# Kernel optimization log

Measured on AMD Instinct MI355X. Metric: run time of the kernel, lower is better.

The kernel has to match this reference:

```python
import jax, jax.numpy as jnp
import numpy as np

B, CIN, COUT, H, W = 8, 64, 64, 128, 128
DG = 1          # deformable groups
K = 9           # 3x3 kernel taps


def conv2d(x, w, b, pad):
    out = jax.lax.conv_general_dilated(
        x, w, window_strides=(1, 1), padding=[(pad, pad), (pad, pad)],
        dimension_numbers=("NCHW", "OIHW", "NCHW"))
    return out + b[None, :, None, None]


def deform_conv2d(x, offset, w, b, dg):
    """torchvision-style DeformConv2d, 3x3, stride 1, pad 1, zeros outside."""
    Bn, Cin, Hn, Wn = x.shape
    Cout = w.shape[0]
    Cg = Cin // dg
    # offset: [B, 2*dg*K, H, W] -> [B, dg, K, 2, H, W] (dy, dx per tap)
    off = offset.reshape(Bn, dg, K, 2, Hn, Wn)
    ky = jnp.repeat(jnp.arange(3) - 1, 3).astype(x.dtype)   # [K]
    kx = jnp.tile(jnp.arange(3) - 1, 3).astype(x.dtype)     # [K]
    base_y = ky[:, None, None] + jnp.arange(Hn, dtype=x.dtype)[None, :, None]  # [K,H,1]
    base_x = kx[:, None, None] + jnp.arange(Wn, dtype=x.dtype)[None, None, :]  # [K,1,W]
    py = base_y[None, None] + off[:, :, :, 0]   # [B,dg,K,H,W]
    px = base_x[None, None] + off[:, :, :, 1]   # [B,dg,K,H,W]

    xg = x.reshape(Bn, dg, Cg, Hn * Wn)         # grouped, flat spatial
    y0 = jnp.floor(py)
    x0 = jnp.floor(px)
    acc = jnp.zeros((Bn, dg, Cg, K * Hn * Wn), dtype=x.dtype)
    for dy in (0, 1):
        for dx in (0, 1):
            yc = y0 + dy
            xc = x0 + dx
            # bilinear corner weight; |py-yc| <= 1 for the 4 corners
            wgt = (1.0 - jnp.abs(py - yc)) * (1.0 - jnp.abs(px - xc))
            valid = (yc >= 0) & (yc < Hn) & (xc >= 0) & (xc < Wn)
            yi = jnp.clip(yc, 0, Hn - 1).astype(jnp.int32)
            xi = jnp.clip(xc, 0, Wn - 1).astype(jnp.int32)
            idx = (yi * Wn + xi).reshape(Bn, dg, 1, -1)          # [B,dg,1,K*H*W]
            v = jnp.take_along_axis(xg, idx, axis=3)             # [B,dg,Cg,K*H*W]
            acc = acc + v * (wgt * valid.astype(x.dtype)).reshape(Bn, dg, 1, -1)
    sampled = acc.reshape(Bn, dg, Cg, K, Hn, Wn)
    wk = w.reshape(Cout, dg, Cg, K)              # [Cout,dg,Cg,K]
    out = jnp.einsum("bgckhw,ogck->bohw", sampled, wk)
    return out + b[None, :, None, None]


def setup_inputs() -> dict:
    key = jax.random.key(0)
    ks = jax.random.split(key, 12)
    s = 0.05  # weight scale to keep activations bounded through the relu stack
    inp = {
        "x": jax.random.normal(ks[0], (B, CIN, H, W), jnp.float32),
        "of": jax.random.normal(ks[1], (B, 2, H, W), jnp.float32),
        "w1": jax.random.normal(ks[2], (CIN, CIN, 3, 3), jnp.float32) * s,
        "b1": jnp.zeros((CIN,), jnp.float32),
        "w2": jax.random.normal(ks[3], (CIN, CIN, 3, 3), jnp.float32) * s,
        "b2": jnp.zeros((CIN,), jnp.float32),
        "w3": jax.random.normal(ks[4], (CIN, CIN, 3, 3), jnp.float32) * s,
        "b3": jnp.zeros((CIN,), jnp.float32),
        "w_off": jax.random.normal(ks[5], (K * DG * 2, 2, 1, 1), jnp.float32) * 0.1,
        "b_off": jnp.zeros((K * DG * 2,), jnp.float32),
        "w_d": jax.random.normal(ks[6], (COUT, CIN, 3, 3), jnp.float32) * s,
        "b_d": jnp.zeros((COUT,), jnp.float32),
    }
    return inp


def reference(x, of, w1, b1, w2, b2, w3, b3, w_off, b_off, w_d, b_d):
    h = jax.nn.relu(conv2d(x, w1, b1, 1))
    h = jax.nn.relu(conv2d(h, w2, b2, 1))
    h = jax.nn.relu(conv2d(h, w3, b3, 1))
    offset = conv2d(of, w_off, b_off, 0)          # 1x1 offset conv -> [B,18*dg,H,W]
    return deform_conv2d(h, offset, w_d, b_d, DG)
```

## Files before the change

kernel.cpp:

```cpp
#include <hip/hip_runtime.h>
#include <math.h>

#define H_ 128
#define W_ 128
#define B_ 8
#define C_ 64
#define HW_ (H_*W_)
#define PW 130

typedef _Float16 half8 __attribute__((ext_vector_type(8)));
typedef _Float16 half4t __attribute__((ext_vector_type(4)));
typedef float f32x4 __attribute__((ext_vector_type(4)));

__device__ __forceinline__ int clampi(int v, int lo, int hi) {
    return v < lo ? lo : (v > hi ? hi : v);
}

__device__ __forceinline__ void stage16(const _Float16* g, _Float16* l) {
    __builtin_amdgcn_global_load_lds(
        (const __attribute__((address_space(1))) unsigned int*)g,
        (__attribute__((address_space(3))) unsigned int*)l, 16, 0, 0);
}

__global__ void wpack_kernel(const float* __restrict__ w1, const float* __restrict__ w2,
                             const float* __restrict__ w3, const float* __restrict__ wd,
                             _Float16* __restrict__ wp) {
    int t = blockIdx.x * 256 + threadIdx.x;
    if (t >= 4 * 4608) return;
    int set = t / 4608;
    int u   = t - set * 4608;
    const float* w = (set == 0) ? w1 : (set == 1) ? w2 : (set == 2) ? w3 : wd;
    int l  = u & 63;
    int mf = (u >> 6) & 3;
    int ch = (u >> 8) & 1;
    int kk = u >> 9;
    int co   = mf * 16 + (l & 15);
    int cin0 = ch * 32 + (l >> 4) * 8;
    half8 v;
#pragma unroll
    for (int j = 0; j < 8; ++j)
        v[j] = (_Float16)w[((co * C_) + cin0 + j) * 9 + kk];
    *(half8*)(wp + (size_t)set * 36864
                 + (size_t)(((ch * 9 + kk) * 4 + mf) * 64 + l) * 8) = v;
}

__global__ __launch_bounds__(256, 4)
void xpad_kernel(const float* __restrict__ x, _Float16* __restrict__ o) {
    __shared__ float lds[64][129];
    const int tid = threadIdx.x;
    const int b = blockIdx.x & 7, y = blockIdx.x >> 3;
    const int xr = tid & 127, cr = tid >> 7;
    const float* src = x + (size_t)b * C_ * HW_ + y * W_;
#pragma unroll
    for (int i = 0; i < 32; ++i) {
        int c = i * 2 + cr;
        lds[c][xr] = src[(size_t)c * HW_ + xr];
    }
    __syncthreads();
    const int px = tid & 127, hf = tid >> 7;
    _Float16* dst = o + ((size_t)((b * PW + y + 1) * PW) + px + 1) * C_ + hf * 32;
#pragma unroll
    for (int q = 0; q < 4; ++q) {
        half8 v;
#pragma unroll
        for (int j = 0; j < 8; ++j) v[j] = (_Float16)lds[hf * 32 + q * 8 + j][px];
        *(half8*)(dst + q * 8) = v;
    }
}

__global__ void zpad_kernel(_Float16* __restrict__ p0, _Float16* __restrict__ p1,
                            _Float16* __restrict__ p2) {
    int t = blockIdx.x * 256 + threadIdx.x;
    if (t >= 3 * B_ * 516) return;
    int which = t / (B_ * 516);
    int u = t - which * (B_ * 516);
    _Float16* o = (which == 0) ? p0 : (which == 1) ? p1 : p2;
    int b = u / 516, i = u % 516;
    int yp, xp;
    if (i < 260) { yp = (i < 130) ? 0 : (PW - 1); xp = i % 130; }
    else {
        int j = i - 260;
        if (j < 128) { xp = 0; yp = j + 1; }
        else         { xp = PW - 1; yp = j - 128 + 1; }
    }
    _Float16* dst = o + ((size_t)(b * PW + yp) * PW + xp) * C_;
    half8 z = (half8)(_Float16)0.f;
#pragma unroll
    for (int c8 = 0; c8 < 8; ++c8) *(half8*)(dst + c8 * 8) = z;
}

__global__ void offconv_kernel(const float* __restrict__ of,
                               const float* __restrict__ w,
                               const float* __restrict__ b,
                               float* __restrict__ out) {
    int bi = blockIdx.x & 7;
    int p  = (blockIdx.x >> 3) * 256 + threadIdx.x;
    float a0 = of[(bi * 2 + 0) * HW_ + p];
    float a1 = of[(bi * 2 + 1) * HW_ + p];
#pragma unroll
    for (int kk = 0; kk < 9; ++kk) {
        float dy = b[2 * kk]     + w[(2 * kk) * 2] * a0     + w[(2 * kk) * 2 + 1] * a1;
        float dx = b[2 * kk + 1] + w[(2 * kk + 1) * 2] * a0 + w[(2 * kk + 1) * 2 + 1] * a1;
        float2 v; v.x = dy; v.y = dx;
        *(float2*)(out + ((size_t)(bi * 9 + kk) * HW_ + p) * 2) = v;
    }
}

__global__ __launch_bounds__(1024, 1)
void conv3x3_mfma(const _Float16* __restrict__ in, const _Float16* __restrict__ wpk,
                  const float* __restrict__ bias, _Float16* __restrict__ outp) {
    __shared__ _Float16 Ash[9 * 4 * 64 * 8];
    __shared__ _Float16 Tile[6 * 4 * 130 * 8];
    const int tid = threadIdx.x;
    const int wv = tid >> 6, l = tid & 63;
    const int l15 = l & 15, lg = l >> 4;
    const int b  = blockIdx.x & 7;
    const int R  = (blockIdx.x >> 3) * 4;
    const int rowi = wv >> 2;
    const int xh = (wv & 3) * 32;

    f32x4 acc[4][2];
#pragma unroll
    for (int i = 0; i < 4; ++i)
#pragma unroll
        for (int j = 0; j < 2; ++j) acc[i][j] = (f32x4){0.f, 0.f, 0.f, 0.f};

    half8 bf0[2], bf1[2];

#define LOADB(BF, KK)                                                          \
    {                                                                          \
        _Pragma("unroll") for (int nf = 0; nf < 2; ++nf)                       \
            BF[nf] = *(const half8*)(Tile + (size_t)(((rowi + (KK) / 3) * 4 + lg) \
                          * 130 + xh + (KK) % 3 + nf * 16 + l15) * 8);         \
    }
#define MM(BF, KK)                                                             \
    {                                                                          \
        half8 af_[4];                                                          \
        _Pragma("unroll") for (int mf = 0; mf < 4; ++mf)                       \
            af_[mf] = *(const half8*)(Ash + (size_t)(((KK) * 4 + mf) * 64 + l) * 8); \
        _Pragma("unroll") for (int mf = 0; mf < 4; ++mf)                       \
            _Pragma("unroll") for (int nf = 0; nf < 2; ++nf)                   \
                acc[mf][nf] = __builtin_amdgcn_mfma_f32_16x16x32_f16(          \
                    af_[mf], BF[nf], acc[mf][nf], 0, 0, 0);                    \
    }

#pragma unroll
    for (int ch = 0; ch < 2; ++ch) {
        __syncthreads();
#pragma unroll
        for (int i = 0; i < 6; ++i) {
            int idx = i * 1024 + tid;
            if (idx < 2304) {
                stage16(wpk + (size_t)ch * 18432 + (size_t)idx * 8,
                        Ash + (size_t)idx * 8);
            } else if (idx < 5424) {
                int t   = idx - 2304;
                int dy  = t / 520;
                int rem = t - dy * 520;
                int pl  = rem / 130;
                int col = rem - pl * 130;
                stage16(in + ((size_t)((b * PW + R + dy) * PW) + col) * C_
                            + ch * 32 + pl * 8,
                        Tile + (size_t)t * 8);
            }
        }
        __syncthreads();

        LOADB(bf0, 0);
        LOADB(bf1, 1); MM(bf0, 0);
        LOADB(bf0, 2); MM(bf1, 1);
        LOADB(bf1, 3); MM(bf0, 2);
        LOADB(bf0, 4); MM(bf1, 3);
        LOADB(bf1, 5); MM(bf0, 4);
        LOADB(bf0, 6); MM(bf1, 5);
        LOADB(bf1, 7); MM(bf0, 6);
        LOADB(bf0, 8); MM(bf1, 7);
                       MM(bf0, 8);
    }
#undef LOADB
#undef MM

    _Float16* ob = outp + ((size_t)((b * PW + R + rowi + 1) * PW) + xh + 1) * C_;
#pragma unroll
    for (int mf = 0; mf < 4; ++mf) {
        const int co = mf * 16 + lg * 4;
        const float b0 = bias[co], b1 = bias[co + 1], b2 = bias[co + 2], b3 = bias[co + 3];
#pragma unroll
        for (int nf = 0; nf < 2; ++nf) {
            f32x4 v = acc[mf][nf];
            half4t h;
            h[0] = (_Float16)fmaxf(v[0] + b0, 0.f);
            h[1] = (_Float16)fmaxf(v[1] + b1, 0.f);
            h[2] = (_Float16)fmaxf(v[2] + b2, 0.f);
            h[3] = (_Float16)fmaxf(v[3] + b3, 0.f);
            *(half4t*)(ob + (nf * 16 + l15) * C_ + co) = h;
        }
    }
}

__global__ __launch_bounds__(1024, 1)
void deform_mfma(const _Float16* __restrict__ hin, const float* __restrict__ off,
                 const _Float16* __restrict__ wpk, const float* __restrict__ bias,
                 float* __restrict__ out) {
    __shared__ _Float16 Ash[9 * 4 * 64 * 8];
    __shared__ _Float16 Win[8 * 130 * 40];
    __shared__ _Float16 OffS[9 * 4 * 128 * 4];
    const int tid = threadIdx.x;
    const int wv = tid >> 6, l = tid & 63;
    const int l15 = l & 15, lg = l >> 4;
    const int b  = blockIdx.x & 7;
    const int R  = (blockIdx.x >> 3) * 4;
    const int r  = R + (wv >> 2);
    const int xh = (wv & 3) * 32;

    const _Float16* hb = hin + (size_t)b * PW * PW * C_;
    const float* offp = off + (size_t)b * 9 * HW_ * 2;

#pragma unroll
    for (int i = 0; i < 3; ++i) {
        int idx = i * 1024 + tid;
        if (idx < 2304) {
            int kk = idx >> 8, rowi = (idx >> 6) & 3, c = idx & 63;
            const _Float16* g = (const _Float16*)(offp
                + ((size_t)kk * HW_ + (R + rowi) * W_) * 2) + c * 8;
            stage16(g, OffS + (size_t)idx * 8);
        }
    }

    f32x4 acc[4][2];
#pragma unroll
    for (int i = 0; i < 4; ++i)
#pragma unroll
        for (int j = 0; j < 2; ++j) acc[i][j] = (f32x4){0.f, 0.f, 0.f, 0.f};

    half8 bf[2];

#define GATHB(KK, CH) do {                                                     \
    _Pragma("unroll") for (int nf = 0; nf < 2; ++nf) {                         \
        const int pxl = xh + nf * 16 + l15;                                    \
        float2 o2 = *(const float2*)(OffS +                                    \
            (size_t)((((KK) * 4 + (r - R)) << 7) + pxl) * 4);                  \
        float py = (float)(r + (KK) / 3 - 1) + o2.x;                           \
        float px = (float)(pxl + (KK) % 3 - 1) + o2.y;                         \
        float fy0 = floorf(py), fx0 = floorf(px);                              \
        float fy = py - fy0, fx = px - fx0;                                    \
        int iy0 = (int)fy0, ix0 = (int)fx0;                                    \
        int cy0 = clampi(iy0, -1, 128), cy1 = clampi(iy0 + 1, -1, 128);        \
        int px0 = clampi(ix0, -1, 128) + 1, px1 = clampi(ix0 + 1, -1, 128) + 1;\
        _Float16 w00 = (_Float16)((1.f - fy) * (1.f - fx));                    \
        _Float16 w01 = (_Float16)((1.f - fy) * fx);                            \
        _Float16 w10 = (_Float16)(fy * (1.f - fx));                            \
        _Float16 w11 = (_Float16)(fy * fx);                                    \
        half8 c0, c1, c2, c3;                                                  \
        int s0 = cy0 + 2 - R, s1 = cy1 + 2 - R;                                \
        if (__all((s0 >= 0) & (s1 <= 7))) {                                    \
            const _Float16* w0 = Win + (size_t)(s0 * 130) * 40 + lg * 8;       \
            const _Float16* w1 = Win + (size_t)(s1 * 130) * 40 + lg * 8;       \
            c0 = *(const half8*)(w0 + px0 * 40);                               \
            c1 = *(const half8*)(w0 + px1 * 40);                               \
            c2 = *(const half8*)(w1 + px0 * 40);                               \
            c3 = *(const half8*)(w1 + px1 * 40);                               \
        } else {                                                               \
            const _Float16* g0 = hb + (size_t)((cy0 + 1) * PW) * C_ + (CH) * 32 + lg * 8; \
            const _Float16* g1 = hb + (size_t)((cy1 + 1) * PW) * C_ + (CH) * 32 + lg * 8; \
            c0 = *(const half8*)(g0 + px0 * C_);                               \
            c1 = *(const half8*)(g0 + px1 * C_);                               \
            c2 = *(const half8*)(g1 + px0 * C_);                               \
            c3 = *(const half8*)(g1 + px1 * C_);                               \
        }                                                                      \
        bf[nf] = (c0 * w00 + c1 * w01) + (c2 * w10 + c3 * w11);                \
    }                                                                          \
} while (0)
#define MMT(KK) do {                                                           \
    half8 af0 = *(const half8*)(Ash + (size_t)(((KK) * 4 + 0) * 64 + l) * 8);  \
    half8 af1 = *(const half8*)(Ash + (size_t)(((KK) * 4 + 1) * 64 + l) * 8);  \
    half8 af2 = *(const half8*)(Ash + (size_t)(((KK) * 4 + 2) * 64 + l) * 8);  \
    half8 af3 = *(const half8*)(Ash + (size_t)(((KK) * 4 + 3) * 64 + l) * 8);  \
    _Pragma("unroll") for (int nf = 0; nf < 2; ++nf) {                         \
        acc[0][nf] = __builtin_amdgcn_mfma_f32_16x16x32_f16(af0, bf[nf], acc[0][nf], 0, 0, 0); \
        acc[1][nf] = __builtin_amdgcn_mfma_f32_16x16x32_f16(af1, bf[nf], acc[1][nf], 0, 0, 0); \
        acc[2][nf] = __builtin_amdgcn_mfma_f32_16x16x32_f16(af2, bf[nf], acc[2][nf], 0, 0, 0); \
        acc[3][nf] = __builtin_amdgcn_mfma_f32_16x16x32_f16(af3, bf[nf], acc[3][nf], 0, 0, 0); \
    }                                                                          \
} while (0)

#pragma unroll
    for (int ch = 0; ch < 2; ++ch) {
        __syncthreads();
#pragma unroll
        for (int i = 0; i < 3; ++i) {
            int idx = i * 1024 + tid;
            if (idx < 2304)
                stage16(wpk + (size_t)ch * 18432 + (size_t)idx * 8,
                        Ash + (size_t)idx * 8);
        }
#pragma unroll
        for (int i = 0; i < 6; ++i) {
            int idx = i * 1024 + tid;
            if (idx < 5200) {
                int s   = idx / 650;
                int rem = idx - s * 650;
                int c   = rem / 5;
                int q   = rem - c * 5;
                int prow = clampi(R - 1 + s, 0, 129);
                stage16(hb + ((size_t)(prow * PW) + c) * C_ + ch * 32 + (q < 4 ? q : 3) * 8,
                        Win + (size_t)idx * 8);
            }
        }
        __syncthreads();

        GATHB(0, ch); MMT(0);
        GATHB(1, ch); MMT(1);
        GATHB(2, ch); MMT(2);
        GATHB(3, ch); MMT(3);
        GATHB(4, ch); MMT(4);
        GATHB(5, ch); MMT(5);
        GATHB(6, ch); MMT(6);
        GATHB(7, ch); MMT(7);
        GATHB(8, ch); MMT(8);
    }
#undef GATHB
#undef MMT

    float* WF = (float*)Win;
    float* obase = out + (size_t)b * C_ * HW_;
#pragma unroll
    for (int p = 0; p < 4; ++p) {
        __syncthreads();
#pragma unroll
        for (int nf = 0; nf < 2; ++nf) {
            f32x4 v = acc[p][nf];
#pragma unroll
            for (int rr = 0; rr < 4; ++rr) {
                int co16 = lg * 4 + rr;
                WF[co16 * 512 + (r - R) * 128 + xh + nf * 16 + l15]
                    = v[rr] + bias[p * 16 + co16];
            }
        }
        __syncthreads();
#pragma unroll
        for (int i = 0; i < 2; ++i) {
            int g4   = i * 1024 + tid;
            int co16 = g4 >> 7;
            int q    = g4 & 127;
            int rr2  = q >> 5;
            int px4  = q & 31;
            f32x4 v = *(const f32x4*)&WF[g4 * 4];
            *(f32x4*)(obase + (size_t)(p * 16 + co16) * HW_ + (R + rr2) * W_ + px4 * 4) = v;
        }
    }
}

extern "C" void kernel_launch(void* const* d_in, const int* in_sizes, int n_in,
                              void* d_out, int out_size, void* d_ws, size_t ws_size,
                              hipStream_t stream) {
    const float* x     = (const float*)d_in[0];
    const float* of    = (const float*)d_in[1];
    const float* w1    = (const float*)d_in[2];
    const float* b1    = (const float*)d_in[3];
    const float* w2    = (const float*)d_in[4];
    const float* b2    = (const float*)d_in[5];
    const float* w3    = (const float*)d_in[6];
    const float* b3    = (const float*)d_in[7];
    const float* w_off = (const float*)d_in[8];
    const float* b_off = (const float*)d_in[9];
    const float* w_d   = (const float*)d_in[10];
    const float* b_d   = (const float*)d_in[11];
    float* out = (float*)d_out;

    char* base = (char*)d_ws;
    float*     offb = (float*)base;
    char* p = base + (size_t)B_ * 18 * HW_ * 4;
    _Float16* wpA = (_Float16*)p;
    _Float16* wp1 = wpA;
    _Float16* wp2 = wp1 + 36864;
    _Float16* wp3 = wp2 + 36864;
    _Float16* wpd = wp3 + 36864;
    p += 4 * 36864 * 2;
    _Float16* xp = (_Float16*)p; p += (size_t)B_ * PW * PW * C_ * 2;
    _Float16* hA = (_Float16*)p; p += (size_t)B_ * PW * PW * C_ * 2;
    _Float16* hB = (_Float16*)p;

    wpack_kernel<<<72, 256, 0, stream>>>(w1, w2, w3, w_d, wpA);
    zpad_kernel<<<(3 * B_ * 516 + 255) / 256, 256, 0, stream>>>(xp, hA, hB);
    xpad_kernel<<<H_ * B_, 256, 0, stream>>>(x, xp);
    offconv_kernel<<<(B_ * HW_) / 256, 256, 0, stream>>>(of, w_off, b_off, offb);

    conv3x3_mfma<<<256, 1024, 0, stream>>>(xp, wp1, b1, hA);
    conv3x3_mfma<<<256, 1024, 0, stream>>>(hA, wp2, b2, hB);
    conv3x3_mfma<<<256, 1024, 0, stream>>>(hB, wp3, b3, hA);
    deform_mfma<<<256, 1024, 0, stream>>>(hA, offb, wpd, b_d, out);
}
```

Baseline: 120.2 us.

## Merge prep kernels into one launch and halve conv block to 512 threads

The four preprocessing kernels (weight pack, pad zeroing, input transpose/pad, offset conv) are merged into a single launch that dispatches on block index. This removes three kernel launches and the gaps between them. Separately, the 3x3 conv kernel now runs 8 waves instead of 16, and each wave computes 64 output columns (4 N-fragments) rather than 32. That gives each wave more MFMA work per A-fragment load at the cost of higher register use and fewer waves to hide latency.

```diff
diff --git a/kernel.cpp b/kernel.cpp
--- a/kernel.cpp
+++ b/kernel.cpp
@@ -22,91 +22,92 @@
         (__attribute__((address_space(3))) unsigned int*)l, 16, 0, 0);
 }
 
-__global__ void wpack_kernel(const float* __restrict__ w1, const float* __restrict__ w2,
-                             const float* __restrict__ w3, const float* __restrict__ wd,
-                             _Float16* __restrict__ wp) {
-    int t = blockIdx.x * 256 + threadIdx.x;
-    if (t >= 4 * 4608) return;
-    int set = t / 4608;
-    int u   = t - set * 4608;
-    const float* w = (set == 0) ? w1 : (set == 1) ? w2 : (set == 2) ? w3 : wd;
-    int l  = u & 63;
-    int mf = (u >> 6) & 3;
-    int ch = (u >> 8) & 1;
-    int kk = u >> 9;
-    int co   = mf * 16 + (l & 15);
-    int cin0 = ch * 32 + (l >> 4) * 8;
-    half8 v;
-#pragma unroll
-    for (int j = 0; j < 8; ++j)
-        v[j] = (_Float16)w[((co * C_) + cin0 + j) * 9 + kk];
-    *(half8*)(wp + (size_t)set * 36864
-                 + (size_t)(((ch * 9 + kk) * 4 + mf) * 64 + l) * 8) = v;
-}
-
 __global__ __launch_bounds__(256, 4)
-void xpad_kernel(const float* __restrict__ x, _Float16* __restrict__ o) {
+void prep_kernel(const float* __restrict__ w1, const float* __restrict__ w2,
+                 const float* __restrict__ w3, const float* __restrict__ wd,
+                 _Float16* __restrict__ wp,
+                 _Float16* __restrict__ z0, _Float16* __restrict__ z1,
+                 _Float16* __restrict__ z2,
+                 const float* __restrict__ x,  _Float16* __restrict__ xp,
+                 const float* __restrict__ of, const float* __restrict__ wof,
+                 const float* __restrict__ bof, float* __restrict__ offb) {
     __shared__ float lds[64][129];
+    const int blk = blockIdx.x;
     const int tid = threadIdx.x;
-    const int b = blockIdx.x & 7, y = blockIdx.x >> 3;
-    const int xr = tid & 127, cr = tid >> 7;
-    const float* src = x + (size_t)b * C_ * HW_ + y * W_;
-#pragma unroll
-    for (int i = 0; i < 32; ++i) {
-        int c = i * 2 + cr;
-        lds[c][xr] = src[(size_t)c * HW_ + xr];
-    }
-    __syncthreads();
-    const int px = tid & 127, hf = tid >> 7;
-    _Float16* dst = o + ((size_t)((b * PW + y + 1) * PW) + px + 1) * C_ + hf * 32;
-#pragma unroll
-    for (int q = 0; q < 4; ++q) {
+
+    if (blk < 72) {
+        int t = blk * 256 + tid;
+        if (t >= 4 * 4608) return;
+        int set = t / 4608;
+        int u   = t - set * 4608;
+        const float* w = (set == 0) ? w1 : (set == 1) ? w2 : (set == 2) ? w3 : wd;
+        int l  = u & 63;
+        int mf = (u >> 6) & 3;
+        int ch = (u >> 8) & 1;
+        int kk = u >> 9;
+        int co   = mf * 16 + (l & 15);
+        int cin0 = ch * 32 + (l >> 4) * 8;
         half8 v;
 #pragma unroll
-        for (int j = 0; j < 8; ++j) v[j] = (_Float16)lds[hf * 32 + q * 8 + j][px];
-        *(half8*)(dst + q * 8) = v;
-    }
-}
-
-__global__ void zpad_kernel(_Float16* __restrict__ p0, _Float16* __restrict__ p1,
-                            _Float16* __restrict__ p2) {
-    int t = blockIdx.x * 256 + threadIdx.x;
-    if (t >= 3 * B_ * 516) return;
-    int which = t / (B_ * 516);
-    int u = t - which * (B_ * 516);
-    _Float16* o = (which == 0) ? p0 : (which == 1) ? p1 : p2;
-    int b = u / 516, i = u % 516;
-    int yp, xp;
-    if (i < 260) { yp = (i < 130) ? 0 : (PW - 1); xp = i % 130; }
-    else {
-        int j = i - 260;
-        if (j < 128) { xp = 0; yp = j + 1; }
-        else         { xp = PW - 1; yp = j - 128 + 1; }
-    }
-    _Float16* dst = o + ((size_t)(b * PW + yp) * PW + xp) * C_;
-    half8 z = (half8)(_Float16)0.f;
-#pragma unroll
-    for (int c8 = 0; c8 < 8; ++c8) *(half8*)(dst + c8 * 8) = z;
-}
-
-__global__ void offconv_kernel(const float* __restrict__ of,
-                               const float* __restrict__ w,
-                               const float* __restrict__ b,
-                               float* __restrict__ out) {
-    int bi = blockIdx.x & 7;
-    int p  = (blockIdx.x >> 3) * 256 + threadIdx.x;
-    float a0 = of[(bi * 2 + 0) * HW_ + p];
-    float a1 = of[(bi * 2 + 1) * HW_ + p];
-#pragma unroll
-    for (int kk = 0; kk < 9; ++kk) {
-        float dy = b[2 * kk]     + w[(2 * kk) * 2] * a0     + w[(2 * kk) * 2 + 1] * a1;
-        float dx = b[2 * kk + 1] + w[(2 * kk + 1) * 2] * a0 + w[(2 * kk + 1) * 2 + 1] * a1;
-        float2 v; v.x = dy; v.y = dx;
-        *(float2*)(out + ((size_t)(bi * 9 + kk) * HW_ + p) * 2) = v;
-    }
-}
-
-__global__ __launch_bounds__(1024, 1)
+        for (int j = 0; j < 8; ++j)
+            v[j] = (_Float16)w[((co * C_) + cin0 + j) * 9 + kk];
+        *(half8*)(wp + (size_t)set * 36864
+                     + (size_t)(((ch * 9 + kk) * 4 + mf) * 64 + l) * 8) = v;
+    } else if (blk < 121) {
+        int t = (blk - 72) * 256 + tid;
+        if (t >= 3 * B_ * 516) return;
+        int which = t / (B_ * 516);
+        int u = t - which * (B_ * 516);
+        _Float16* o = (which == 0) ? z0 : (which == 1) ? z1 : z2;
+        int b = u / 516, i = u % 516;
+        int yp, xpx;
+        if (i < 260) { yp = (i < 130) ? 0 : (PW - 1); xpx = i % 130; }
+        else {
+            int j = i - 260;
+            if (j < 128) { xpx = 0; yp = j + 1; }
+            else         { xpx = PW - 1; yp = j - 128 + 1; }
+        }
+        _Float16* dst = o + ((size_t)(b * PW + yp) * PW + xpx) * C_;
+        half8 z = (half8)(_Float16)0.f;
+#pragma unroll
+        for (int c8 = 0; c8 < 8; ++c8) *(half8*)(dst + c8 * 8) = z;
+    } else if (blk < 1145) {
+        int bb = blk - 121;
+        const int b = bb & 7, y = bb >> 3;
+        const int xr = tid & 127, cr = tid >> 7;
+        const float* src = x + (size_t)b * C_ * HW_ + y * W_;
+#pragma unroll
+        for (int i = 0; i < 32; ++i) {
+            int c = i * 2 + cr;
+            lds[c][xr] = src[(size_t)c * HW_ + xr];
+        }
+        __syncthreads();
+        const int px = tid & 127, hf = tid >> 7;
+        _Float16* dst = xp + ((size_t)((b * PW + y + 1) * PW) + px + 1) * C_ + hf * 32;
+#pragma unroll
+        for (int q = 0; q < 4; ++q) {
+            half8 v;
+#pragma unroll
+            for (int j = 0; j < 8; ++j) v[j] = (_Float16)lds[hf * 32 + q * 8 + j][px];
+            *(half8*)(dst + q * 8) = v;
+        }
+    } else {
+        int bb = blk - 1145;
+        int bi = bb & 7;
+        int p  = (bb >> 3) * 256 + tid;
+        float a0 = of[(bi * 2 + 0) * HW_ + p];
+        float a1 = of[(bi * 2 + 1) * HW_ + p];
+#pragma unroll
+        for (int kk = 0; kk < 9; ++kk) {
+            float dy = bof[2 * kk]     + wof[(2 * kk) * 2] * a0     + wof[(2 * kk) * 2 + 1] * a1;
+            float dx = bof[2 * kk + 1] + wof[(2 * kk + 1) * 2] * a0 + wof[(2 * kk + 1) * 2 + 1] * a1;
+            float2 v; v.x = dy; v.y = dx;
+            *(float2*)(offb + ((size_t)(bi * 9 + kk) * HW_ + p) * 2) = v;
+        }
+    }
+}
+
+__global__ __launch_bounds__(512, 1)
 void conv3x3_mfma(const _Float16* __restrict__ in, const _Float16* __restrict__ wpk,
                   const float* __restrict__ bias, _Float16* __restrict__ outp) {
     __shared__ _Float16 Ash[9 * 4 * 64 * 8];
@@ -116,22 +117,22 @@
     const int l15 = l & 15, lg = l >> 4;
     const int b  = blockIdx.x & 7;
     const int R  = (blockIdx.x >> 3) * 4;
-    const int rowi = wv >> 2;
-    const int xh = (wv & 3) * 32;
-
-    f32x4 acc[4][2];
+    const int rowi = wv >> 1;
+    const int xcol = (wv & 1) * 64;
+
+    f32x4 acc[4][4];
 #pragma unroll
     for (int i = 0; i < 4; ++i)
 #pragma unroll
-        for (int j = 0; j < 2; ++j) acc[i][j] = (f32x4){0.f, 0.f, 0.f, 0.f};
-
-    half8 bf0[2], bf1[2];
+        for (int j = 0; j < 4; ++j) acc[i][j] = (f32x4){0.f, 0.f, 0.f, 0.f};
+
+    half8 bf0[4], bf1[4];
 
 #define LOADB(BF, KK)                                                          \
     {                                                                          \
-        _Pragma("unroll") for (int nf = 0; nf < 2; ++nf)                       \
+        _Pragma("unroll") for (int nf = 0; nf < 4; ++nf)                       \
             BF[nf] = *(const half8*)(Tile + (size_t)(((rowi + (KK) / 3) * 4 + lg) \
-                          * 130 + xh + (KK) % 3 + nf * 16 + l15) * 8);         \
+                          * 130 + xcol + (KK) % 3 + nf * 16 + l15) * 8);       \
     }
 #define MM(BF, KK)                                                             \
     {                                                                          \
@@ -139,7 +140,7 @@
         _Pragma("unroll") for (int mf = 0; mf < 4; ++mf)                       \
             af_[mf] = *(const half8*)(Ash + (size_t)(((KK) * 4 + mf) * 64 + l) * 8); \
         _Pragma("unroll") for (int mf = 0; mf < 4; ++mf)                       \
-            _Pragma("unroll") for (int nf = 0; nf < 2; ++nf)                   \
+            _Pragma("unroll") for (int nf = 0; nf < 4; ++nf)                   \
                 acc[mf][nf] = __builtin_amdgcn_mfma_f32_16x16x32_f16(          \
                     af_[mf], BF[nf], acc[mf][nf], 0, 0, 0);                    \
     }
@@ -148,8 +149,8 @@
     for (int ch = 0; ch < 2; ++ch) {
         __syncthreads();
 #pragma unroll
-        for (int i = 0; i < 6; ++i) {
-            int idx = i * 1024 + tid;
+        for (int i = 0; i < 11; ++i) {
+            int idx = i * 512 + tid;
             if (idx < 2304) {
                 stage16(wpk + (size_t)ch * 18432 + (size_t)idx * 8,
                         Ash + (size_t)idx * 8);
@@ -180,13 +181,13 @@
 #undef LOADB
 #undef MM
 
-    _Float16* ob = outp + ((size_t)((b * PW + R + rowi + 1) * PW) + xh + 1) * C_;
+    _Float16* ob = outp + ((size_t)((b * PW + R + rowi + 1) * PW) + xcol + 1) * C_;
 #pragma unroll
     for (int mf = 0; mf < 4; ++mf) {
         const int co = mf * 16 + lg * 4;
         const float b0 = bias[co], b1 = bias[co + 1], b2 = bias[co + 2], b3 = bias[co + 3];
 #pragma unroll
-        for (int nf = 0; nf < 2; ++nf) {
+        for (int nf = 0; nf < 4; ++nf) {
             f32x4 v = acc[mf][nf];
             half4t h;
             h[0] = (_Float16)fmaxf(v[0] + b0, 0.f);
@@ -381,13 +382,12 @@
     _Float16* hA = (_Float16*)p; p += (size_t)B_ * PW * PW * C_ * 2;
     _Float16* hB = (_Float16*)p;
 
-    wpack_kernel<<<72, 256, 0, stream>>>(w1, w2, w3, w_d, wpA);
-    zpad_kernel<<<(3 * B_ * 516 + 255) / 256, 256, 0, stream>>>(xp, hA, hB);
-    xpad_kernel<<<H_ * B_, 256, 0, stream>>>(x, xp);
-    offconv_kernel<<<(B_ * HW_) / 256, 256, 0, stream>>>(of, w_off, b_off, offb);
-
-    conv3x3_mfma<<<256, 1024, 0, stream>>>(xp, wp1, b1, hA);
-    conv3x3_mfma<<<256, 1024, 0, stream>>>(hA, wp2, b2, hB);
-    conv3x3_mfma<<<256, 1024, 0, stream>>>(hB, wp3, b3, hA);
+    prep_kernel<<<1657, 256, 0, stream>>>(w1, w2, w3, w_d, wpA,
+                                          xp, hA, hB,
+                                          x, xp, of, w_off, b_off, offb);
+
+    conv3x3_mfma<<<256, 512, 0, stream>>>(xp, wp1, b1, hA);
+    conv3x3_mfma<<<256, 512, 0, stream>>>(hA, wp2, b2, hB);
+    conv3x3_mfma<<<256, 512, 0, stream>>>(hB, wp3, b3, hA);
     deform_mfma<<<256, 1024, 0, stream>>>(hA, offb, wpd, b_d, out);
 }
```

New measurement: 106.6 us. 11.3% less time.

## Fuse all stages into one cooperative persistent kernel with grid syncs

Applied to the files above, without the earlier changes.

Replaces the eight separate launches (weight pack, padding, transpose, offset conv, three convs, deform conv) with a single cooperative kernel of 256 blocks that runs each stage as a device function separated by grid.sync(). Shared memory is one union buffer reused across phases. This removes launch gaps and inter-kernel drain between the short stages. In exchange it depends on all 256 blocks of 1024 threads being co-resident, adds grid-wide barrier costs, and may change register allocation for the fused code.

```diff
diff --git a/kernel.cpp b/kernel.cpp
--- a/kernel.cpp
+++ b/kernel.cpp
@@ -1,5 +1,8 @@
 #include <hip/hip_runtime.h>
+#include <hip/hip_cooperative_groups.h>
 #include <math.h>
+
+namespace cg = cooperative_groups;
 
 #define H_ 128
 #define W_ 128
@@ -22,100 +25,14 @@
         (__attribute__((address_space(3))) unsigned int*)l, 16, 0, 0);
 }
 
-__global__ void wpack_kernel(const float* __restrict__ w1, const float* __restrict__ w2,
-                             const float* __restrict__ w3, const float* __restrict__ wd,
-                             _Float16* __restrict__ wp) {
-    int t = blockIdx.x * 256 + threadIdx.x;
-    if (t >= 4 * 4608) return;
-    int set = t / 4608;
-    int u   = t - set * 4608;
-    const float* w = (set == 0) ? w1 : (set == 1) ? w2 : (set == 2) ? w3 : wd;
-    int l  = u & 63;
-    int mf = (u >> 6) & 3;
-    int ch = (u >> 8) & 1;
-    int kk = u >> 9;
-    int co   = mf * 16 + (l & 15);
-    int cin0 = ch * 32 + (l >> 4) * 8;
-    half8 v;
-#pragma unroll
-    for (int j = 0; j < 8; ++j)
-        v[j] = (_Float16)w[((co * C_) + cin0 + j) * 9 + kk];
-    *(half8*)(wp + (size_t)set * 36864
-                 + (size_t)(((ch * 9 + kk) * 4 + mf) * 64 + l) * 8) = v;
-}
-
-__global__ __launch_bounds__(256, 4)
-void xpad_kernel(const float* __restrict__ x, _Float16* __restrict__ o) {
-    __shared__ float lds[64][129];
-    const int tid = threadIdx.x;
-    const int b = blockIdx.x & 7, y = blockIdx.x >> 3;
-    const int xr = tid & 127, cr = tid >> 7;
-    const float* src = x + (size_t)b * C_ * HW_ + y * W_;
-#pragma unroll
-    for (int i = 0; i < 32; ++i) {
-        int c = i * 2 + cr;
-        lds[c][xr] = src[(size_t)c * HW_ + xr];
-    }
-    __syncthreads();
-    const int px = tid & 127, hf = tid >> 7;
-    _Float16* dst = o + ((size_t)((b * PW + y + 1) * PW) + px + 1) * C_ + hf * 32;
-#pragma unroll
-    for (int q = 0; q < 4; ++q) {
-        half8 v;
-#pragma unroll
-        for (int j = 0; j < 8; ++j) v[j] = (_Float16)lds[hf * 32 + q * 8 + j][px];
-        *(half8*)(dst + q * 8) = v;
-    }
-}
-
-__global__ void zpad_kernel(_Float16* __restrict__ p0, _Float16* __restrict__ p1,
-                            _Float16* __restrict__ p2) {
-    int t = blockIdx.x * 256 + threadIdx.x;
-    if (t >= 3 * B_ * 516) return;
-    int which = t / (B_ * 516);
-    int u = t - which * (B_ * 516);
-    _Float16* o = (which == 0) ? p0 : (which == 1) ? p1 : p2;
-    int b = u / 516, i = u % 516;
-    int yp, xp;
-    if (i < 260) { yp = (i < 130) ? 0 : (PW - 1); xp = i % 130; }
-    else {
-        int j = i - 260;
-        if (j < 128) { xp = 0; yp = j + 1; }
-        else         { xp = PW - 1; yp = j - 128 + 1; }
-    }
-    _Float16* dst = o + ((size_t)(b * PW + yp) * PW + xp) * C_;
-    half8 z = (half8)(_Float16)0.f;
-#pragma unroll
-    for (int c8 = 0; c8 < 8; ++c8) *(half8*)(dst + c8 * 8) = z;
-}
-
-__global__ void offconv_kernel(const float* __restrict__ of,
-                               const float* __restrict__ w,
-                               const float* __restrict__ b,
-                               float* __restrict__ out) {
-    int bi = blockIdx.x & 7;
-    int p  = (blockIdx.x >> 3) * 256 + threadIdx.x;
-    float a0 = of[(bi * 2 + 0) * HW_ + p];
-    float a1 = of[(bi * 2 + 1) * HW_ + p];
-#pragma unroll
-    for (int kk = 0; kk < 9; ++kk) {
-        float dy = b[2 * kk]     + w[(2 * kk) * 2] * a0     + w[(2 * kk) * 2 + 1] * a1;
-        float dx = b[2 * kk + 1] + w[(2 * kk + 1) * 2] * a0 + w[(2 * kk + 1) * 2 + 1] * a1;
-        float2 v; v.x = dy; v.y = dx;
-        *(float2*)(out + ((size_t)(bi * 9 + kk) * HW_ + p) * 2) = v;
-    }
-}
-
-__global__ __launch_bounds__(1024, 1)
-void conv3x3_mfma(const _Float16* __restrict__ in, const _Float16* __restrict__ wpk,
-                  const float* __restrict__ bias, _Float16* __restrict__ outp) {
-    __shared__ _Float16 Ash[9 * 4 * 64 * 8];
-    __shared__ _Float16 Tile[6 * 4 * 130 * 8];
-    const int tid = threadIdx.x;
+__device__ __forceinline__ void conv_phase(
+    const _Float16* __restrict__ in, const _Float16* __restrict__ wpk,
+    const float* __restrict__ bias, _Float16* __restrict__ outp,
+    _Float16* Ash, _Float16* Tile, int blk, int tid) {
     const int wv = tid >> 6, l = tid & 63;
     const int l15 = l & 15, lg = l >> 4;
-    const int b  = blockIdx.x & 7;
-    const int R  = (blockIdx.x >> 3) * 4;
+    const int b  = blk & 7;
+    const int R  = (blk >> 3) * 4;
     const int rowi = wv >> 2;
     const int xh = (wv & 3) * 32;
 
@@ -196,20 +113,18 @@
             *(half4t*)(ob + (nf * 16 + l15) * C_ + co) = h;
         }
     }
-}
-
-__global__ __launch_bounds__(1024, 1)
-void deform_mfma(const _Float16* __restrict__ hin, const float* __restrict__ off,
-                 const _Float16* __restrict__ wpk, const float* __restrict__ bias,
-                 float* __restrict__ out) {
-    __shared__ _Float16 Ash[9 * 4 * 64 * 8];
-    __shared__ _Float16 Win[8 * 130 * 40];
-    __shared__ _Float16 OffS[9 * 4 * 128 * 4];
-    const int tid = threadIdx.x;
+    __syncthreads();
+}
+
+__device__ __forceinline__ void deform_phase(
+    const _Float16* __restrict__ hin, const float* __restrict__ off,
+    const _Float16* __restrict__ wpk, const float* __restrict__ bias,
+    float* __restrict__ out,
+    _Float16* Ash, _Float16* Win, _Float16* OffS, int blk, int tid) {
     const int wv = tid >> 6, l = tid & 63;
     const int l15 = l & 15, lg = l >> 4;
-    const int b  = blockIdx.x & 7;
-    const int R  = (blockIdx.x >> 3) * 4;
+    const int b  = blk & 7;
+    const int R  = (blk >> 3) * 4;
     const int r  = R + (wv >> 2);
     const int xh = (wv & 3) * 32;
 
@@ -351,6 +266,111 @@
     }
 }
 
+__global__ __launch_bounds__(1024, 1)
+void fused_kernel(const float* __restrict__ x,  const float* __restrict__ of,
+                  const float* __restrict__ w1, const float* __restrict__ w2,
+                  const float* __restrict__ w3, const float* __restrict__ wd,
+                  const float* __restrict__ wof, const float* __restrict__ bof,
+                  const float* __restrict__ b1, const float* __restrict__ b2,
+                  const float* __restrict__ b3, const float* __restrict__ bd,
+                  float* __restrict__ out, float* __restrict__ offb,
+                  _Float16* __restrict__ wpA, _Float16* __restrict__ xp,
+                  _Float16* __restrict__ hA, _Float16* __restrict__ hB) {
+    cg::grid_group grid = cg::this_grid();
+    __shared__ long long Ubuf[19616];
+    _Float16* U = (_Float16*)Ubuf;
+    const int blk = blockIdx.x, tid = threadIdx.x;
+
+    {
+        int T = blk * 1024 + tid;
+        if (T < 131072) {
+            int bi = T >> 14, p = T & 16383;
+            float a0 = of[(bi * 2 + 0) * HW_ + p];
+            float a1 = of[(bi * 2 + 1) * HW_ + p];
+#pragma unroll
+            for (int kk = 0; kk < 9; ++kk) {
+                float dy = bof[2 * kk]     + wof[(2 * kk) * 2] * a0     + wof[(2 * kk) * 2 + 1] * a1;
+                float dx = bof[2 * kk + 1] + wof[(2 * kk + 1) * 2] * a0 + wof[(2 * kk + 1) * 2 + 1] * a1;
+                float2 v; v.x = dy; v.y = dx;
+                *(float2*)(offb + ((size_t)(bi * 9 + kk) * HW_ + p) * 2) = v;
+            }
+        } else if (T < 149504) {
+            int u4 = T - 131072;
+            int set = u4 / 4608;
+            int u   = u4 - set * 4608;
+            const float* w = (set == 0) ? w1 : (set == 1) ? w2 : (set == 2) ? w3 : wd;
+            int l  = u & 63;
+            int mf = (u >> 6) & 3;
+            int ch = (u >> 8) & 1;
+            int kk = u >> 9;
+            int co   = mf * 16 + (l & 15);
+            int cin0 = ch * 32 + (l >> 4) * 8;
+            half8 v;
+#pragma unroll
+            for (int j = 0; j < 8; ++j)
+                v[j] = (_Float16)w[((co * C_) + cin0 + j) * 9 + kk];
+            *(half8*)(wpA + (size_t)set * 36864
+                          + (size_t)(((ch * 9 + kk) * 4 + mf) * 64 + l) * 8) = v;
+        } else if (T < 161888) {
+            int u0 = T - 149504;
+            int which = u0 / (B_ * 516);
+            int u = u0 - which * (B_ * 516);
+            _Float16* o = (which == 0) ? xp : (which == 1) ? hA : hB;
+            int b = u / 516, i = u % 516;
+            int yp, xpx;
+            if (i < 260) { yp = (i < 130) ? 0 : (PW - 1); xpx = i % 130; }
+            else {
+                int j = i - 260;
+                if (j < 128) { xpx = 0; yp = j + 1; }
+                else         { xpx = PW - 1; yp = j - 128 + 1; }
+            }
+            _Float16* dst = o + ((size_t)(b * PW + yp) * PW + xpx) * C_;
+            half8 z = (half8)(_Float16)0.f;
+#pragma unroll
+            for (int c8 = 0; c8 < 8; ++c8) *(half8*)(dst + c8 * 8) = z;
+        }
+        {
+            float* ldsx = (float*)Ubuf + (size_t)(tid >> 8) * (64 * 129);
+            int rt = blk * 4 + (tid >> 8);
+            int b = rt & 7, y = rt >> 3;
+            int t2 = tid & 255;
+            const int xr = t2 & 127, cr = t2 >> 7;
+            const float* src = x + (size_t)b * C_ * HW_ + y * W_;
+#pragma unroll
+            for (int i = 0; i < 32; ++i) {
+                int c = i * 2 + cr;
+                ldsx[c * 129 + xr] = src[(size_t)c * HW_ + xr];
+            }
+            __syncthreads();
+            const int px = t2 & 127, hf = t2 >> 7;
+            _Float16* dst = xp + ((size_t)((b * PW + y + 1) * PW) + px + 1) * C_ + hf * 32;
+#pragma unroll
+            for (int q = 0; q < 4; ++q) {
+                half8 v;
+#pragma unroll
+                for (int j = 0; j < 8; ++j)
+                    v[j] = (_Float16)ldsx[(hf * 32 + q * 8 + j) * 129 + px];
+                *(half8*)(dst + q * 8) = v;
+            }
+        }
+    }
+    grid.sync();
+
+    _Float16* AshC  = U;
+    _Float16* TileC = U + 18432;
+    _Float16* AshD  = U;
+    _Float16* WinD  = U + 18432;
+    _Float16* OffSD = U + 18432 + 41600;
+
+    conv_phase(xp, wpA,             b1, hA, AshC, TileC, blk, tid);
+    grid.sync();
+    conv_phase(hA, wpA + 36864,     b2, hB, AshC, TileC, blk, tid);
+    grid.sync();
+    conv_phase(hB, wpA + 2 * 36864, b3, hA, AshC, TileC, blk, tid);
+    grid.sync();
+    deform_phase(hA, offb, wpA + 3 * 36864, bd, out, AshD, WinD, OffSD, blk, tid);
+}
+
 extern "C" void kernel_launch(void* const* d_in, const int* in_sizes, int n_in,
                               void* d_out, int out_size, void* d_ws, size_t ws_size,
                               hipStream_t stream) {
@@ -372,22 +392,17 @@
     float*     offb = (float*)base;
     char* p = base + (size_t)B_ * 18 * HW_ * 4;
     _Float16* wpA = (_Float16*)p;
-    _Float16* wp1 = wpA;
-    _Float16* wp2 = wp1 + 36864;
-    _Float16* wp3 = wp2 + 36864;
-    _Float16* wpd = wp3 + 36864;
     p += 4 * 36864 * 2;
     _Float16* xp = (_Float16*)p; p += (size_t)B_ * PW * PW * C_ * 2;
     _Float16* hA = (_Float16*)p; p += (size_t)B_ * PW * PW * C_ * 2;
     _Float16* hB = (_Float16*)p;
 
-    wpack_kernel<<<72, 256, 0, stream>>>(w1, w2, w3, w_d, wpA);
-    zpad_kernel<<<(3 * B_ * 516 + 255) / 256, 256, 0, stream>>>(xp, hA, hB);
-    xpad_kernel<<<H_ * B_, 256, 0, stream>>>(x, xp);
-    offconv_kernel<<<(B_ * HW_) / 256, 256, 0, stream>>>(of, w_off, b_off, offb);
-
-    conv3x3_mfma<<<256, 1024, 0, stream>>>(xp, wp1, b1, hA);
-    conv3x3_mfma<<<256, 1024, 0, stream>>>(hA, wp2, b2, hB);
-    conv3x3_mfma<<<256, 1024, 0, stream>>>(hB, wp3, b3, hA);
-    deform_mfma<<<256, 1024, 0, stream>>>(hA, offb, wpd, b_d, out);
-}
+    void* args[] = {
+        (void*)&x, (void*)&of, (void*)&w1, (void*)&w2, (void*)&w3, (void*)&w_d,
+        (void*)&w_off, (void*)&b_off, (void*)&b1, (void*)&b2, (void*)&b3,
+        (void*)&b_d, (void*)&out, (void*)&offb, (void*)&wpA, (void*)&xp,
+        (void*)&hA, (void*)&hB
+    };
+    hipLaunchCooperativeKernel((void*)fused_kernel, dim3(256), dim3(1024),
+                               args, 0, stream);
+}
```

After: 255.4 us. +112.5%, slower.
